# Performance work log

Hardware: AMD Instinct MI355X
Metric: run time of the kernel (lower is better)

The kernel has to match this reference:

```python
import jax, jax.numpy as jnp
import numpy as np

TOP_K = 2
NUM_EXPERTS = 8
D_MODEL = 1024
G, S = 8, 2048


def setup_inputs() -> dict:
    key = jax.random.key(0)
    k1, k2 = jax.random.split(key)
    x = jax.random.normal(k1, (G, S, D_MODEL), dtype=jnp.float32)
    # orthogonal init approximated by scaled normal (same distributional scale);
    gate_weight = jax.random.normal(k2, (D_MODEL, NUM_EXPERTS), dtype=jnp.float32) * (1.0 / np.sqrt(D_MODEL))
    gate_bias = jnp.zeros((1, 1, NUM_EXPERTS), dtype=jnp.float32)
    return {"x": x, "gate_weight": gate_weight, "gate_bias": gate_bias, "expert_capacity": 256}


def reference(x, gate_weight, gate_bias, expert_capacity):
    # gating: (g,s,d) @ (d,e) -> (g,s,e)
    gating_logits = jnp.einsum('gsd,de->gse', x, gate_weight) + gate_bias
    gating_probs = jax.nn.softmax(gating_logits, axis=-1)
    # eval path: exact top-k over experts
    expert_gate, expert_index = jax.lax.top_k(gating_probs, TOP_K)  # (g,s,t)
    expert_mask = jax.nn.one_hot(expert_index, NUM_EXPERTS, dtype=gating_probs.dtype)  # (g,s,t,e)
    # running position of each token within each expert's buffer (1-indexed where assigned)
    position_in_expert = jnp.cumsum(expert_mask, axis=1) * expert_mask  # (g,s,t,e)
    valid_assignment = (position_in_expert < expert_capacity).astype(expert_gate.dtype)
    expert_gate_valid = expert_gate[..., None] * valid_assignment  # (g,s,t,e)
    # one-hot over capacity slots: (g,s,t,e,c)
    slot_one_hot = jax.nn.one_hot(position_in_expert, expert_capacity, dtype=gating_probs.dtype)
    combine_per_assignment = expert_gate_valid[..., None] * slot_one_hot
    combine_tensor = jnp.sum(combine_per_assignment, axis=2)  # contract over t: (g,s,e,c)
    combine_tensor = combine_tensor[..., 1:]  # drop slot 0 (= unassigned)
    dispatch_mask = combine_tensor.astype(bool)
    return (combine_tensor, dispatch_mask)
```

## Files before the change

### kernel.cpp

```cpp
#include <hip/hip_runtime.h>

#define G 8
#define S 2048
#define DMODEL 1024
#define NE 8
#define TOKENS (G * S)

__global__ __launch_bounds__(64) void gate_topk_kernel(
    const float* __restrict__ x, const float* __restrict__ W,
    const float* __restrict__ bias,
    int* __restrict__ idx01, float* __restrict__ g0out,
    float* __restrict__ g1out) {
  const int lane = threadIdx.x;
  const int tok0 = blockIdx.x * 8;

  const float4* W4 = (const float4*)W;
  float4 wa[16], wb[16];
#pragma unroll
  for (int c = 0; c < 16; ++c) {
    int d = lane + (c << 6);
    wa[c] = W4[d * 2];
    wb[c] = W4[d * 2 + 1];
  }
  float b[8];
#pragma unroll
  for (int e = 0; e < 8; ++e) b[e] = bias[e];

  for (int t = 0; t < 8; ++t) {
    const int tok = tok0 + t;
    const float* xp = x + (size_t)tok * DMODEL;
    float acc[8] = {0.f, 0.f, 0.f, 0.f, 0.f, 0.f, 0.f, 0.f};
#pragma unroll
    for (int c = 0; c < 16; ++c) {
      float xv = xp[lane + (c << 6)];
      acc[0] = fmaf(xv, wa[c].x, acc[0]);
      acc[1] = fmaf(xv, wa[c].y, acc[1]);
      acc[2] = fmaf(xv, wa[c].z, acc[2]);
      acc[3] = fmaf(xv, wa[c].w, acc[3]);
      acc[4] = fmaf(xv, wb[c].x, acc[4]);
      acc[5] = fmaf(xv, wb[c].y, acc[5]);
      acc[6] = fmaf(xv, wb[c].z, acc[6]);
      acc[7] = fmaf(xv, wb[c].w, acc[7]);
    }
#pragma unroll
    for (int e = 0; e < 8; ++e) {
      float v = acc[e];
#pragma unroll
      for (int off = 1; off < 64; off <<= 1) v += __shfl_xor(v, off);
      acc[e] = v + b[e];
    }
    if (lane == 0) {
      float m = acc[0];
#pragma unroll
      for (int e = 1; e < 8; ++e) m = fmaxf(m, acc[e]);
      float p[8], sum = 0.f;
#pragma unroll
      for (int e = 0; e < 8; ++e) {
        p[e] = __expf(acc[e] - m);
        sum += p[e];
      }
      int i0 = 0;
      float best = acc[0];
#pragma unroll
      for (int e = 1; e < 8; ++e)
        if (acc[e] > best) { best = acc[e]; i0 = e; }
      int i1 = -1;
      float b1 = 0.f;
#pragma unroll
      for (int e = 0; e < 8; ++e) {
        if (e == i0) continue;
        if (i1 < 0 || acc[e] > b1) { b1 = acc[e]; i1 = e; }
      }
      float inv = 1.0f / sum;
      idx01[tok] = i0 | (i1 << 8);
      g0out[tok] = p[i0] * inv;
      g1out[tok] = p[i1] * inv;
    }
  }
}

__global__ __launch_bounds__(256) void scan_kernel(
    const int* __restrict__ idx01, int* __restrict__ pos0,
    int* __restrict__ pos1) {
  const int g = blockIdx.x;
  const int t = threadIdx.x;
  const int lane = t & 63;
  const int wave = t >> 6;
  const int base = g * S + t * 8;

  int loc[8];
  unsigned long long a0 = 0ULL, a1 = 0ULL, b0 = 0ULL, b1 = 0ULL;
#pragma unroll
  for (int i = 0; i < 8; ++i) {
    int v = idx01[base + i];
    loc[i] = v;
    int i0 = v & 0xFF, i1 = (v >> 8) & 0xFF;
    if (i0 < 4) a0 += 1ULL << (16 * i0); else a1 += 1ULL << (16 * (i0 & 3));
    if (i1 < 4) b0 += 1ULL << (16 * i1); else b1 += 1ULL << (16 * (i1 & 3));
  }
  const unsigned long long la0 = a0, la1 = a1, lb0 = b0, lb1 = b1;

#pragma unroll
  for (int off = 1; off < 64; off <<= 1) {
    unsigned long long u0 = __shfl_up(a0, (unsigned)off);
    unsigned long long u1 = __shfl_up(a1, (unsigned)off);
    unsigned long long u2 = __shfl_up(b0, (unsigned)off);
    unsigned long long u3 = __shfl_up(b1, (unsigned)off);
    if (lane >= off) { a0 += u0; a1 += u1; b0 += u2; b1 += u3; }
  }

  __shared__ unsigned long long wt[4][4];
  if (lane == 63) {
    wt[wave][0] = a0; wt[wave][1] = a1; wt[wave][2] = b0; wt[wave][3] = b1;
  }
  __syncthreads();
  for (int w = 0; w < wave; ++w) {
    a0 += wt[w][0]; a1 += wt[w][1]; b0 += wt[w][2]; b1 += wt[w][3];
  }

  a0 -= la0; a1 -= la1; b0 -= lb0; b1 -= lb1;

#pragma unroll
  for (int i = 0; i < 8; ++i) {
    int v = loc[i];
    int i0 = v & 0xFF, i1 = (v >> 8) & 0xFF;
    int p0, p1;
    {
      int sh = 16 * (i0 & 3);
      if (i0 < 4) { p0 = (int)((a0 >> sh) & 0xFFFF) + 1; a0 += 1ULL << sh; }
      else        { p0 = (int)((a1 >> sh) & 0xFFFF) + 1; a1 += 1ULL << sh; }
    }
    {
      int sh = 16 * (i1 & 3);
      if (i1 < 4) { p1 = (int)((b0 >> sh) & 0xFFFF) + 1; b0 += 1ULL << sh; }
      else        { p1 = (int)((b1 >> sh) & 0xFFFF) + 1; b1 += 1ULL << sh; }
    }
    pos0[base + i] = p0;
    pos1[base + i] = p1;
  }
}

__global__ __launch_bounds__(256) void fill_kernel(
    const int* __restrict__ idx01, const int* __restrict__ pos0,
    const int* __restrict__ pos1, const float* __restrict__ g0,
    const float* __restrict__ g1, float* __restrict__ combine,
    float* __restrict__ dispatch, int slots) {
  const int tid = blockIdx.x * 256 + threadIdx.x;
  const int wid = tid >> 6;
  const int lane = tid & 63;
  const int e = wid & 7;
  const int tok = wid >> 3;

  const int v = idx01[tok];
  const int i0 = v & 0xFF, i1 = (v >> 8) & 0xFF;
  int target = -1;
  float gate = 0.f;
  if (e == i0) {
    int p = pos0[tok];
    if (p <= slots) { target = p - 1; gate = g0[tok]; }
  } else if (e == i1) {
    int p = pos1[tok];
    if (p <= slots) { target = p - 1; gate = g1[tok]; }
  }
  const bool hit_valid = (gate != 0.f);

  const size_t base = (size_t)wid * (size_t)slots;
#pragma unroll
  for (int c = 0; c < 4; ++c) {
    int slot = lane + (c << 6);
    if (slot < slots) {
      bool hit = (slot == target);
      combine[base + slot] = hit ? gate : 0.f;
      dispatch[base + slot] = (hit && hit_valid) ? 1.f : 0.f;
    }
  }
}

extern "C" void kernel_launch(void* const* d_in, const int* in_sizes, int n_in,
                              void* d_out, int out_size, void* d_ws,
                              size_t ws_size, hipStream_t stream) {
  const float* x = (const float*)d_in[0];
  const float* W = (const float*)d_in[1];
  const float* bias = (const float*)d_in[2];

  float* out = (float*)d_out;
  const int rows = TOKENS * NE;
  const int slots = out_size / (2 * rows);
  float* combine = out;
  float* dispatch = out + (size_t)(out_size / 2);

  char* ws = (char*)d_ws;
  int* idx01 = (int*)(ws + 0);
  float* g0 = (float*)(ws + TOKENS * 4);
  float* g1 = (float*)(ws + TOKENS * 8);
  int* pos0 = (int*)(ws + TOKENS * 12);
  int* pos1 = (int*)(ws + TOKENS * 16);

  gate_topk_kernel<<<TOKENS / 8, 64, 0, stream>>>(x, W, bias, idx01, g0, g1);
  scan_kernel<<<G, 256, 0, stream>>>(idx01, pos0, pos1);
  fill_kernel<<<(rows * 64) / 256, 256, 0, stream>>>(idx01, pos0, pos1, g0, g1,
                                                     combine, dispatch, slots);
}
```

Before: 345.6 us.

## Vectorize gate loads and fill output with flat float4 stores from per-row metadata

The gating kernel now reads x as float4 and assigns each lane four contiguous d indices, re-laying out W to match. The scan kernel now emits a per-(token, expert) int2 holding target slot and gate, so the fill kernel no longer reads idx/pos/gate arrays separately. The fill kernel switches from one wave per row with scalar stores to a grid-stride loop writing float4 chunks over the flat output, with each chunk possibly straddling two rows. It hardcodes 255 slots per row, so it breaks if the capacity differs, and dispatch is derived from combine being nonzero.

```diff
diff --git a/kernel.cpp b/kernel.cpp
--- a/kernel.cpp
+++ b/kernel.cpp
@@ -15,12 +15,15 @@
   const int tok0 = blockIdx.x * 8;
 
   const float4* W4 = (const float4*)W;
-  float4 wa[16], wb[16];
-#pragma unroll
-  for (int c = 0; c < 16; ++c) {
-    int d = lane + (c << 6);
-    wa[c] = W4[d * 2];
-    wb[c] = W4[d * 2 + 1];
+  float4 wa[4][4], wb[4][4];
+#pragma unroll
+  for (int c = 0; c < 4; ++c) {
+#pragma unroll
+    for (int j = 0; j < 4; ++j) {
+      int d = 4 * (lane + (c << 6)) + j;
+      wa[c][j] = W4[d * 2];
+      wb[c][j] = W4[d * 2 + 1];
+    }
   }
   float b[8];
 #pragma unroll
@@ -28,19 +31,24 @@
 
   for (int t = 0; t < 8; ++t) {
     const int tok = tok0 + t;
-    const float* xp = x + (size_t)tok * DMODEL;
+    const float4* xp = (const float4*)(x + (size_t)tok * DMODEL);
     float acc[8] = {0.f, 0.f, 0.f, 0.f, 0.f, 0.f, 0.f, 0.f};
 #pragma unroll
-    for (int c = 0; c < 16; ++c) {
-      float xv = xp[lane + (c << 6)];
-      acc[0] = fmaf(xv, wa[c].x, acc[0]);
-      acc[1] = fmaf(xv, wa[c].y, acc[1]);
-      acc[2] = fmaf(xv, wa[c].z, acc[2]);
-      acc[3] = fmaf(xv, wa[c].w, acc[3]);
-      acc[4] = fmaf(xv, wb[c].x, acc[4]);
-      acc[5] = fmaf(xv, wb[c].y, acc[5]);
-      acc[6] = fmaf(xv, wb[c].z, acc[6]);
-      acc[7] = fmaf(xv, wb[c].w, acc[7]);
+    for (int c = 0; c < 4; ++c) {
+      float4 xv = xp[lane + (c << 6)];
+      const float xs[4] = {xv.x, xv.y, xv.z, xv.w};
+#pragma unroll
+      for (int j = 0; j < 4; ++j) {
+        float s = xs[j];
+        acc[0] = fmaf(s, wa[c][j].x, acc[0]);
+        acc[1] = fmaf(s, wa[c][j].y, acc[1]);
+        acc[2] = fmaf(s, wa[c][j].z, acc[2]);
+        acc[3] = fmaf(s, wa[c][j].w, acc[3]);
+        acc[4] = fmaf(s, wb[c][j].x, acc[4]);
+        acc[5] = fmaf(s, wb[c][j].y, acc[5]);
+        acc[6] = fmaf(s, wb[c][j].z, acc[6]);
+        acc[7] = fmaf(s, wb[c][j].w, acc[7]);
+      }
     }
 #pragma unroll
     for (int e = 0; e < 8; ++e) {
@@ -79,9 +87,9 @@
   }
 }
 
-__global__ __launch_bounds__(256) void scan_kernel(
-    const int* __restrict__ idx01, int* __restrict__ pos0,
-    int* __restrict__ pos1) {
+__global__ __launch_bounds__(256) void scan_meta_kernel(
+    const int* __restrict__ idx01, const float* __restrict__ g0,
+    const float* __restrict__ g1, int2* __restrict__ meta, int slots) {
   const int g = blockIdx.x;
   const int t = threadIdx.x;
   const int lane = t & 63;
@@ -122,6 +130,7 @@
 
 #pragma unroll
   for (int i = 0; i < 8; ++i) {
+    const int tok = base + i;
     int v = loc[i];
     int i0 = v & 0xFF, i1 = (v >> 8) & 0xFF;
     int p0, p1;
@@ -135,44 +144,55 @@
       if (i1 < 4) { p1 = (int)((b0 >> sh) & 0xFFFF) + 1; b0 += 1ULL << sh; }
       else        { p1 = (int)((b1 >> sh) & 0xFFFF) + 1; b1 += 1ULL << sh; }
     }
-    pos0[base + i] = p0;
-    pos1[base + i] = p1;
+    const float G0 = g0[tok], G1 = g1[tok];
+    int2* mrow = meta + (size_t)tok * NE;
+#pragma unroll
+    for (int e = 0; e < 8; ++e) {
+      int tgt = -1;
+      float gv = 0.f;
+      if (e == i0) {
+        if (p0 <= slots) { tgt = p0 - 1; gv = G0; }
+      } else if (e == i1) {
+        if (p1 <= slots) { tgt = p1 - 1; gv = G1; }
+      }
+      mrow[e] = make_int2(tgt, __float_as_int(gv));
+    }
   }
 }
 
 __global__ __launch_bounds__(256) void fill_kernel(
-    const int* __restrict__ idx01, const int* __restrict__ pos0,
-    const int* __restrict__ pos1, const float* __restrict__ g0,
-    const float* __restrict__ g1, float* __restrict__ combine,
-    float* __restrict__ dispatch, int slots) {
-  const int tid = blockIdx.x * 256 + threadIdx.x;
-  const int wid = tid >> 6;
-  const int lane = tid & 63;
-  const int e = wid & 7;
-  const int tok = wid >> 3;
-
-  const int v = idx01[tok];
-  const int i0 = v & 0xFF, i1 = (v >> 8) & 0xFF;
-  int target = -1;
-  float gate = 0.f;
-  if (e == i0) {
-    int p = pos0[tok];
-    if (p <= slots) { target = p - 1; gate = g0[tok]; }
-  } else if (e == i1) {
-    int p = pos1[tok];
-    if (p <= slots) { target = p - 1; gate = g1[tok]; }
-  }
-  const bool hit_valid = (gate != 0.f);
-
-  const size_t base = (size_t)wid * (size_t)slots;
-#pragma unroll
-  for (int c = 0; c < 4; ++c) {
-    int slot = lane + (c << 6);
-    if (slot < slots) {
-      bool hit = (slot == target);
-      combine[base + slot] = hit ? gate : 0.f;
-      dispatch[base + slot] = (hit && hit_valid) ? 1.f : 0.f;
-    }
+    const int2* __restrict__ meta, float* __restrict__ combine,
+    float* __restrict__ dispatch, int nchunks, int total_rows, int slots) {
+  const int stride = gridDim.x * 256;
+  for (int idx = blockIdx.x * 256 + threadIdx.x; idx < nchunks; idx += stride) {
+    const unsigned f = (unsigned)idx * 4u;
+    const unsigned row = __umulhi(f, 0x80808081u) >> 7;
+    const int sb = (int)(f - row * 255u);
+    const int2 mA = meta[row];
+    unsigned rB = row + 1u;
+    if ((int)rB >= total_rows) rB = row;
+    const int2 mB = meta[rB];
+    const int ta = mA.x, tb = mB.x;
+    const float ga = __int_as_float(mA.y), gb = __int_as_float(mB.y);
+
+    float4 cv;
+    {
+      int s0 = sb + 0;
+      cv.x = (s0 < 255) ? ((s0 == ta) ? ga : 0.f) : ((s0 - 255 == tb) ? gb : 0.f);
+      int s1 = sb + 1;
+      cv.y = (s1 < 255) ? ((s1 == ta) ? ga : 0.f) : ((s1 - 255 == tb) ? gb : 0.f);
+      int s2 = sb + 2;
+      cv.z = (s2 < 255) ? ((s2 == ta) ? ga : 0.f) : ((s2 - 255 == tb) ? gb : 0.f);
+      int s3 = sb + 3;
+      cv.w = (s3 < 255) ? ((s3 == ta) ? ga : 0.f) : ((s3 - 255 == tb) ? gb : 0.f);
+    }
+    ((float4*)combine)[idx] = cv;
+    float4 dv;
+    dv.x = (cv.x != 0.f) ? 1.f : 0.f;
+    dv.y = (cv.y != 0.f) ? 1.f : 0.f;
+    dv.z = (cv.z != 0.f) ? 1.f : 0.f;
+    dv.w = (cv.w != 0.f) ? 1.f : 0.f;
+    ((float4*)dispatch)[idx] = dv;
   }
 }
 
@@ -193,11 +213,13 @@
   int* idx01 = (int*)(ws + 0);
   float* g0 = (float*)(ws + TOKENS * 4);
   float* g1 = (float*)(ws + TOKENS * 8);
-  int* pos0 = (int*)(ws + TOKENS * 12);
-  int* pos1 = (int*)(ws + TOKENS * 16);
+  int2* meta = (int2*)(ws + TOKENS * 12);
+
+  const int ndwords = rows * slots;
+  const int nchunks = ndwords >> 2;
 
   gate_topk_kernel<<<TOKENS / 8, 64, 0, stream>>>(x, W, bias, idx01, g0, g1);
-  scan_kernel<<<G, 256, 0, stream>>>(idx01, pos0, pos1);
-  fill_kernel<<<(rows * 64) / 256, 256, 0, stream>>>(idx01, pos0, pos1, g0, g1,
-                                                     combine, dispatch, slots);
-}
+  scan_meta_kernel<<<G, 256, 0, stream>>>(idx01, g0, g1, meta, slots);
+  fill_kernel<<<2048, 256, 0, stream>>>(meta, combine, dispatch, nchunks, rows,
+                                        slots);
+}
```

Result: faster. 335.0 us (-3.0%).
